# Optimization experiments

Measured on AMD Instinct MI355X. Metric: run time of the kernel, lower is better.

Reference implementation:

```python
import jax, jax.numpy as jnp
import numpy as np

# dims (match init_kwargs)
T, B, N, D_OB = 256, 32, 64, 4
D_MODEL = N * D_OB            # 256
D_PE = 16
D_T = D_MODEL + D_PE          # 272 transformer width
H = 8
DH = D_T // H                 # 34
L = 2
DFF = 1024
C = 2
MAX_LEN = T
F_IN = T * D_OB               # 1024, ObservationPropagation channels


def setup_inputs() -> dict:
    key = jax.random.key(0)
    ks = jax.random.split(key, 24)
    g = lambda k, shp: 0.02 * jax.random.normal(k, shp, dtype=jnp.float32)
    return {
        "x": jax.random.normal(ks[0], (T, B, N), dtype=jnp.float32),
        "times": jnp.sort(jax.random.uniform(ks[1], (T, B), dtype=jnp.float32) * MAX_LEN, axis=0),
        "lengths": jax.random.randint(ks[2], (B,), MAX_LEN // 2, MAX_LEN + 1),
        "R_u": g(ks[3], (1, N * D_OB)),
        "Wv1": g(ks[4], (F_IN, F_IN)), "bv1": g(ks[5], (F_IN,)),
        "Wv2": g(ks[6], (F_IN, F_IN)), "bv2": g(ks[7], (F_IN,)),
        "qkv_w": g(ks[8], (L, D_T, 3 * D_T)), "qkv_b": g(ks[9], (L, 3 * D_T)),
        "out_w": g(ks[10], (L, D_T, D_T)), "out_b": g(ks[11], (L, D_T)),
        "ln1_w": jnp.ones((L, D_T), jnp.float32), "ln1_b": jnp.zeros((L, D_T), jnp.float32),
        "ln2_w": jnp.ones((L, D_T), jnp.float32), "ln2_b": jnp.zeros((L, D_T), jnp.float32),
        "ffn_w1": g(ks[12], (L, D_T, DFF)), "ffn_b1": g(ks[13], (L, DFF)),
        "ffn_w2": g(ks[14], (L, DFF, D_T)), "ffn_b2": g(ks[15], (L, D_T)),
        "mlp_w1": g(ks[16], (D_T, D_T)), "mlp_b1": g(ks[17], (D_T,)),
        "mlp_w2": g(ks[18], (D_T, C)), "mlp_b2": g(ks[19], (C,)),
    }


def _pos_encode(times):
    # PositionalEncodingTF: timescales = max_len ** linspace(0,1,d_pe//2)
    scales = MAX_LEN ** np.linspace(0.0, 1.0, D_PE // 2)
    st = times[..., None] / jnp.asarray(scales, times.dtype)  # [T,B,8]
    return jnp.concatenate([jnp.sin(st), jnp.cos(st)], axis=-1)  # [T,B,16]


def _segment_softmax(w, seg, num_segments):
    m = jax.ops.segment_max(w, seg, num_segments=num_segments)
    e = jnp.exp(w - m[seg])
    s = jax.ops.segment_sum(e, seg, num_segments=num_segments)
    return e / s[seg]


def _ob_propagate(xn, src, tgt, edge_w, Wv, bv):
    """Batched ObservationPropagation (use_beta=False, decompose=False).
    xn: [B,N,F]; messages = relu(lin_value(x_src)) * softmax(edge_w per target);
    scatter-add at targets. Returns (out, pre-softmax alpha == edge_w)."""
    gamma = _segment_softmax(edge_w, tgt, N)              # [E]
    value = jax.nn.relu(xn @ Wv + bv)                     # [B,N,F] (linear commutes with gather)
    msg = value[:, src, :] * gamma[None, :, None]         # [B,E,F] -- dominant memory traffic
    out = jnp.zeros_like(xn).at[:, tgt, :].add(msg)       # segment-sum at target nodes
    return out, edge_w


def _ln(x, w, b):
    mu = jnp.mean(x, axis=-1, keepdims=True)
    var = jnp.mean((x - mu) ** 2, axis=-1, keepdims=True)
    return (x - mu) / jnp.sqrt(var + 1e-5) * w + b


def _encoder_layer(xt, key_pad, qkv_w, qkv_b, out_w, out_b, ln1_w, ln1_b, ln2_w, ln2_b, w1, b1, w2, b2):
    # xt: [T,B,D_T]; key_pad: [B,T] True = padded. Post-norm torch TransformerEncoderLayer, relu, no dropout.
    Tt, Bb, _ = xt.shape
    q, k, v = jnp.split(xt @ qkv_w + qkv_b, 3, axis=-1)
    to_h = lambda t: t.reshape(Tt, Bb, H, DH).transpose(1, 2, 0, 3)  # [B,H,T,dh]
    scores = jnp.einsum("bhqd,bhkd->bhqk", to_h(q), to_h(k)) / jnp.sqrt(jnp.asarray(DH, xt.dtype))
    scores = jnp.where(key_pad[:, None, None, :], -jnp.inf, scores)
    attn = jax.nn.softmax(scores, axis=-1)
    o = jnp.einsum("bhqk,bhkd->bhqd", attn, to_h(v)).transpose(2, 0, 1, 3).reshape(Tt, Bb, D_T)
    xt = _ln(xt + o @ out_w + out_b, ln1_w, ln1_b)
    ff = jax.nn.relu(xt @ w1 + b1) @ w2 + b2
    return _ln(xt + ff, ln2_w, ln2_b)


def _forward(x, times, lengths, R_u, Wv1, bv1, Wv2, bv2, qkv_w, qkv_b, out_w, out_b,
             ln1_w, ln1_b, ln2_w, ln2_b, ffn_w1, ffn_b1, ffn_w2, ffn_b2,
             mlp_w1, mlp_b1, mlp_w2, mlp_b2):
    Bb = x.shape[1]
    # observation embedding: repeat each sensor d_ob times, scale by R_u, relu
    h = jax.nn.relu(jnp.repeat(x, D_OB, axis=-1) * R_u)          # [T,B,N*d_ob]
    pe = _pos_encode(times)                                      # [T,B,16]
    key_pad = jnp.arange(T)[None, :] >= lengths[:, None]         # [B,T]
    # reshape to per-sensor node features: [B, N, T*d_ob]
    xn = h.reshape(T, Bb, N, D_OB).transpose(1, 2, 0, 3).reshape(Bb, N, F_IN)
    # dense all-pairs graph (global_structure = ones); torch.nonzero order is row-major
    src = jnp.repeat(jnp.arange(N), N)   # edge_index[0]
    tgt = jnp.tile(jnp.arange(N), N)     # edge_index[1] (aggregation index)
    ew = jnp.ones((N * N,), x.dtype)
    xn, ew2 = _ob_propagate(xn, src, tgt, ew, Wv1, bv1)
    xn, _ = _ob_propagate(xn, src, tgt, ew2, Wv2, bv2)
    out = xn.reshape(Bb, N, T, D_OB).transpose(2, 0, 1, 3).reshape(T, Bb, N * D_OB)
    out = jnp.concatenate([out, pe], axis=2)                     # [T,B,272]
    for l in range(L):
        out = _encoder_layer(out, key_pad, qkv_w[l], qkv_b[l], out_w[l], out_b[l],
                             ln1_w[l], ln1_b[l], ln2_w[l], ln2_b[l],
                             ffn_w1[l], ffn_b1[l], ffn_w2[l], ffn_b2[l])
    keep = (~key_pad).T[:, :, None].astype(out.dtype)            # [T,B,1]
    agg = jnp.sum(out * keep, axis=0) / (lengths[:, None].astype(out.dtype) + 1.0)
    hid = jax.nn.relu(agg @ mlp_w1 + mlp_b1)
    logits = hid @ mlp_w2 + mlp_b2
    return jax.nn.softmax(logits, axis=1)                        # [B,C]


def reference(x, times, lengths, R_u, Wv1, bv1, Wv2, bv2, qkv_w, qkv_b, out_w, out_b,
              ln1_w, ln1_b, ln2_w, ln2_b, ffn_w1, ffn_b1, ffn_w2, ffn_b2,
              mlp_w1, mlp_b1, mlp_w2, mlp_b2):
    return _forward(x, times, lengths, R_u, Wv1, bv1, Wv2, bv2, qkv_w, qkv_b, out_w, out_b,
                    ln1_w, ln1_b, ln2_w, ln2_b, ffn_w1, ffn_b1, ffn_w2, ffn_b2,
                    mlp_w1, mlp_b1, mlp_w2, mlp_b2)
```

## Files before the change

### kernel.cpp

```cpp
#include <hip/hip_runtime.h>
#include <math.h>

#define T_DIM 256
#define B_DIM 32
#define N_DIM 64
#define F_INF 1024
#define D_T 272
#define H_DIM 8
#define DH_DIM 34
#define DFF_DIM 1024

typedef unsigned int uint;
typedef short bf16x8 __attribute__((ext_vector_type(8)));
typedef float f32x4 __attribute__((ext_vector_type(4)));

__device__ __forceinline__ ushort f2bf(float f) {
    uint u = __float_as_uint(f);
    uint r = (u + 0x7fffu + ((u >> 16) & 1u)) >> 16;
    return (ushort)r;
}
__device__ __forceinline__ float bf2f(ushort u) {
    return __uint_as_float(((uint)u) << 16);
}

__global__ void xn_kernel(const float* __restrict__ x, const float* __restrict__ Ru,
                          ushort* __restrict__ xn) {
    int idx = blockIdx.x * blockDim.x + threadIdx.x;
    if (idx >= B_DIM * N_DIM * F_INF) return;
    int f = idx & 1023;
    int bn = idx >> 10;
    int n = bn & 63;
    int b = bn >> 6;
    int t = f >> 2;
    int d = f & 3;
    float v = x[(t * B_DIM + b) * N_DIM + n] * Ru[(n << 2) + d];
    xn[idx] = f2bf(fmaxf(v, 0.0f));
}

struct WT {
    int tstart[11];
    const float* src[10];
    ushort* dst[10];
    int K[10];
    int N[10];
    int ntn[10];
};
__global__ __launch_bounds__(256) void wconv_tiled(WT s) {
    int tile = blockIdx.x;
    int seg = 0;
    while (seg < 9 && tile >= s.tstart[seg + 1]) ++seg;
    int ti = tile - s.tstart[seg];
    int ntn = s.ntn[seg];
    int tk = ti / ntn, tn = ti - tk * ntn;
    int K = s.K[seg], N = s.N[seg];
    __shared__ float t[16][17];
    int ty = threadIdx.x >> 4, tx = threadIdx.x & 15;
    t[ty][tx] = s.src[seg][(size_t)(tk * 16 + ty) * N + tn * 16 + tx];
    __syncthreads();
    s.dst[seg][(size_t)(tn * 16 + ty) * K + tk * 16 + tx] = f2bf(t[tx][ty]);
}

template <int ACT, int OUT_MODE>
__global__ __launch_bounds__(256) void gemm_mfma(const ushort* __restrict__ A,
                                                 const ushort* __restrict__ Bt,
                                                 const float* __restrict__ bias,
                                                 void* __restrict__ Cout,
                                                 int M, int N, int K) {
    __shared__ ushort As[2][64 * 32];
    __shared__ ushort Bs[2][128 * 32];
    const int tid = threadIdx.x;
    const int m0 = blockIdx.y * 64;
    const int n0 = blockIdx.x * 128;
    const int w = tid >> 6, lane = tid & 63;
    const int wr = w >> 1, wc = w & 1;
    const int lr = lane & 15, lk = lane >> 4;

    const int nfull = K >> 5;
    const int ns = (K + 31) >> 5;

    const int ra = w * 16 + (lane >> 2);
    const int ca = (((lane & 3) ^ ((ra >> 1) & 3)) << 3);
    int gma = m0 + ra; if (gma > M - 1) gma = M - 1;
    const ushort* gA = &A[(size_t)gma * K + ca];
    const int rb0 = w * 32 + (lane >> 2);
    const int cb0 = (((lane & 3) ^ ((rb0 >> 1) & 3)) << 3);
    const int rb1 = rb0 + 16;
    const int cb1 = (((lane & 3) ^ ((rb1 >> 1) & 3)) << 3);
    int gnb0 = n0 + rb0; if (gnb0 > N - 1) gnb0 = N - 1;
    int gnb1 = n0 + rb1; if (gnb1 > N - 1) gnb1 = N - 1;
    const ushort* gB0 = &Bt[(size_t)gnb0 * K + cb0];
    const ushort* gB1 = &Bt[(size_t)gnb1 * K + cb1];

    f32x4 acc[2][4];
#pragma unroll
    for (int i = 0; i < 2; ++i)
#pragma unroll
        for (int j = 0; j < 4; ++j) acc[i][j] = (f32x4){0.f, 0.f, 0.f, 0.f};

    auto stage = [&](int buf, int s) {
        const int k0 = s << 5;
        if (s < nfull) {
            __builtin_amdgcn_global_load_lds(
                (const __attribute__((address_space(1))) void*)(gA + k0),
                (__attribute__((address_space(3))) void*)(&As[buf][w * 512]), 16, 0, 0);
            __builtin_amdgcn_global_load_lds(
                (const __attribute__((address_space(1))) void*)(gB0 + k0),
                (__attribute__((address_space(3))) void*)(&Bs[buf][w * 1024]), 16, 0, 0);
            __builtin_amdgcn_global_load_lds(
                (const __attribute__((address_space(1))) void*)(gB1 + k0),
                (__attribute__((address_space(3))) void*)(&Bs[buf][w * 1024 + 512]), 16, 0, 0);
        } else {
            {
                int r = tid >> 2, p = tid & 3;
                int g = p ^ ((r >> 1) & 3);
                int gm = m0 + r; if (gm > M - 1) gm = M - 1;
                ushort v[8];
#pragma unroll
                for (int e = 0; e < 8; ++e) {
                    int gk = k0 + g * 8 + e;
                    v[e] = (gk < K) ? A[(size_t)gm * K + gk] : (ushort)0;
                }
                *reinterpret_cast<uint4*>(&As[buf][r * 32 + p * 8]) =
                    *reinterpret_cast<uint4*>(v);
            }
#pragma unroll
            for (int rr = 0; rr < 2; ++rr) {
                int r = rr * 64 + (tid >> 2), p = tid & 3;
                int g = p ^ ((r >> 1) & 3);
                int gn = n0 + r; if (gn > N - 1) gn = N - 1;
                ushort v[8];
#pragma unroll
                for (int e = 0; e < 8; ++e) {
                    int gk = k0 + g * 8 + e;
                    v[e] = (gk < K) ? Bt[(size_t)gn * K + gk] : (ushort)0;
                }
                *reinterpret_cast<uint4*>(&Bs[buf][r * 32 + p * 8]) =
                    *reinterpret_cast<uint4*>(v);
            }
        }
    };

    stage(0, 0);
    asm volatile("s_waitcnt vmcnt(0) lgkmcnt(0)" ::: "memory");
    __builtin_amdgcn_sched_barrier(0);
    __builtin_amdgcn_s_barrier();
    __builtin_amdgcn_sched_barrier(0);

    int cur = 0;
    for (int s = 0; s < ns; ++s) {
        if (s + 1 < ns) stage(cur ^ 1, s + 1);

        bf16x8 af[2], bf[4];
#pragma unroll
        for (int mt = 0; mt < 2; ++mt) {
            int row = wr * 32 + mt * 16 + lr;
            int ch = lk ^ ((row >> 1) & 3);
            af[mt] = *reinterpret_cast<const bf16x8*>(&As[cur][row * 32 + ch * 8]);
        }
#pragma unroll
        for (int nt = 0; nt < 4; ++nt) {
            int row = wc * 64 + nt * 16 + lr;
            int ch = lk ^ ((row >> 1) & 3);
            bf[nt] = *reinterpret_cast<const bf16x8*>(&Bs[cur][row * 32 + ch * 8]);
        }
        __builtin_amdgcn_s_setprio(1);
#pragma unroll
        for (int mt = 0; mt < 2; ++mt)
#pragma unroll
            for (int nt = 0; nt < 4; ++nt)
                acc[mt][nt] = __builtin_amdgcn_mfma_f32_16x16x32_bf16(
                    af[mt], bf[nt], acc[mt][nt], 0, 0, 0);
        __builtin_amdgcn_s_setprio(0);

        if (s + 1 < ns) {
            asm volatile("s_waitcnt vmcnt(0) lgkmcnt(0)" ::: "memory");
            __builtin_amdgcn_sched_barrier(0);
            __builtin_amdgcn_s_barrier();
            __builtin_amdgcn_sched_barrier(0);
        }
        cur ^= 1;
    }

#pragma unroll
    for (int nt = 0; nt < 4; ++nt) {
        int col = n0 + wc * 64 + nt * 16 + lr;
        if (col >= N) continue;
        float bv = bias[col];
        int g = 0, dcol = 0;
        if (OUT_MODE == 2) { g = col / 34; dcol = col - g * 34; }
#pragma unroll
        for (int mt = 0; mt < 2; ++mt) {
#pragma unroll
            for (int r = 0; r < 4; ++r) {
                int row = m0 + wr * 32 + mt * 16 + lk * 4 + r;
                if (row >= M) continue;
                float v = acc[mt][nt][r] + bv;
                if (ACT == 1) v = fmaxf(v, 0.0f);
                if (OUT_MODE == 0)
                    ((float*)Cout)[(size_t)row * N + col] = v;
                else if (OUT_MODE == 1)
                    ((ushort*)Cout)[(size_t)row * N + col] = f2bf(v);
                else
                    ((ushort*)Cout)[(size_t)row * 960 + g * 40 + dcol] = f2bf(v);
            }
        }
    }
}

__global__ __launch_bounds__(256) void reduce_s1_kernel(const ushort* __restrict__ val1,
                                                        ushort* __restrict__ s1) {
    int idx = blockIdx.x * 256 + threadIdx.x;
    if (idx >= B_DIM * 128) return;
    int b = idx >> 7;
    int g0 = (idx & 127) << 3;
    const ushort* base = val1 + (size_t)(b << 6) * F_INF + g0;
    float s[8] = {0.f, 0.f, 0.f, 0.f, 0.f, 0.f, 0.f, 0.f};
    for (int n = 0; n < 64; ++n) {
        bf16x8 v = *reinterpret_cast<const bf16x8*>(base + (size_t)n * F_INF);
#pragma unroll
        for (int e = 0; e < 8; ++e) s[e] += bf2f((ushort)v[e]);
    }
    ushort o[8];
#pragma unroll
    for (int e = 0; e < 8; ++e) o[e] = f2bf(s[e] * (1.0f / 64.0f));
    *reinterpret_cast<uint4*>(&s1[(size_t)idx * 8]) = *reinterpret_cast<uint4*>(o);
}

__global__ void seq_kernel(const float* __restrict__ out2, const float* __restrict__ times,
                           ushort* __restrict__ seq) {
    int idx = blockIdx.x * blockDim.x + threadIdx.x;
    if (idx >= T_DIM * B_DIM * D_T) return;
    int c = idx % D_T;
    int tb = idx / D_T;
    float v;
    if (c < 256) {
        v = out2[(tb % B_DIM) * 1024 + ((tb / B_DIM) << 2) + (c & 3)];
    } else {
        int s = c - 256;
        int sc = (s < 8) ? s : s - 8;
        float arg = times[tb] * exp2f(-8.0f * (float)sc * (1.0f / 7.0f));
        v = (s < 8) ? sinf(arg) : cosf(arg);
    }
    seq[idx] = f2bf(v);
}

__global__ void pad_zero_kernel(uint* __restrict__ qkvb) {
    int idx = blockIdx.x * blockDim.x + threadIdx.x;
    if (idx >= T_DIM * B_DIM * 24 * 3) return;
    int row = idx / 72;
    int r = idx - row * 72;
    int g = r / 3, q = r - g * 3;
    qkvb[(size_t)row * 480 + g * 20 + 17 + q] = 0;
}

__global__ __launch_bounds__(256) void attn_mfma(const ushort* __restrict__ qkv,
                                                 const int* __restrict__ lengths,
                                                 ushort* __restrict__ attno) {
    const int b = blockIdx.x >> 3;
    const int h = blockIdx.x & 7;
    const int tid = threadIdx.x;
    const int w = tid >> 6, lane = tid & 63;
    const int lr = lane & 15, lk = lane >> 4;
    __shared__ ushort Ks[2][64 * 40];
    __shared__ ushort Vt[2][48 * 72];
    __shared__ ushort Ps[4][64 * 72];
    const int len = lengths[b];
    const float scale = 0.1714985851f;
    const bf16x8 zv = {0, 0, 0, 0, 0, 0, 0, 0};

    for (int i = tid; i < 2 * 8 * 72; i += 256) {
        int bb = i / 576;
        Vt[bb][40 * 72 + (i - bb * 576)] = 0;
    }

    const int srow0 = tid / 5, sch0 = tid - srow0 * 5;
    const int srow1 = (tid + 256) / 5, sch1 = (tid + 256) - srow1 * 5;
    const int sjp0 = (srow0 & 15) * 4 + (srow0 >> 4);
    const int sjp1 = (srow1 & 15) * 4 + (srow1 >> 4);
    const bool has1 = (tid < 64);
    bf16x8 kreg0, kreg1, vreg0, vreg1;

    auto LOADS = [&](int c) {
        const ushort* b0 = &qkv[(size_t)((c * 64 + srow0) * 32 + b) * 960 + h * 40];
        kreg0 = *reinterpret_cast<const bf16x8*>(b0 + 320 + sch0 * 8);
        vreg0 = *reinterpret_cast<const bf16x8*>(b0 + 640 + sch0 * 8);
        if (has1) {
            const ushort* b1 = &qkv[(size_t)((c * 64 + srow1) * 32 + b) * 960 + h * 40];
            kreg1 = *reinterpret_cast<const bf16x8*>(b1 + 320 + sch1 * 8);
            vreg1 = *reinterpret_cast<const bf16x8*>(b1 + 640 + sch1 * 8);
        }
    };
    auto WRITES = [&](int buf) {
        *reinterpret_cast<bf16x8*>(&Ks[buf][srow0 * 40 + sch0 * 8]) = kreg0;
#pragma unroll
        for (int e = 0; e < 8; ++e) Vt[buf][(sch0 * 8 + e) * 72 + sjp0] = (ushort)vreg0[e];
        if (has1) {
            *reinterpret_cast<bf16x8*>(&Ks[buf][srow1 * 40 + sch1 * 8]) = kreg1;
#pragma unroll
            for (int e = 0; e < 8; ++e) Vt[buf][(sch1 * 8 + e) * 72 + sjp1] = (ushort)vreg1[e];
        }
    };

    bf16x8 qf0[4], qf1[4];
#pragma unroll
    for (int it = 0; it < 4; ++it) {
        int t = w * 64 + it * 16 + lr;
        const ushort* qrow = &qkv[(size_t)(t * 32 + b) * 960 + h * 40];
        qf0[it] = *reinterpret_cast<const bf16x8*>(qrow + lk * 8);
        qf1[it] = (lk == 0) ? *reinterpret_cast<const bf16x8*>(qrow + 32) : zv;
    }

    f32x4 oacc[4][3];
#pragma unroll
    for (int it = 0; it < 4; ++it)
#pragma unroll
        for (int dt = 0; dt < 3; ++dt) oacc[it][dt] = (f32x4){0.f, 0.f, 0.f, 0.f};
    float m[4][4], l[4][4];
#pragma unroll
    for (int it = 0; it < 4; ++it)
#pragma unroll
        for (int r = 0; r < 4; ++r) { m[it][r] = -1e30f; l[it][r] = 0.f; }

    const int nchunks = (len + 63) >> 6;
    LOADS(0);
    WRITES(0);
    __syncthreads();

    int cur = 0;
    for (int c = 0; c < nchunks; ++c) {
        const bool pre = (c + 1 < nchunks);
        if (pre) LOADS(c + 1);

        bf16x8 kf0[4], kf1[4];
#pragma unroll
        for (int jt = 0; jt < 4; ++jt) {
            int j = jt * 16 + lr;
            kf0[jt] = *reinterpret_cast<const bf16x8*>(&Ks[cur][j * 40 + lk * 8]);
            kf1[jt] = (lk == 0) ? *reinterpret_cast<const bf16x8*>(&Ks[cur][j * 40 + 32]) : zv;
        }

        const bool tail = (c * 64 + 64 > len);
#pragma unroll
        for (int it = 0; it < 4; ++it) {
            f32x4 sacc[4];
#pragma unroll
            for (int jt = 0; jt < 4; ++jt) sacc[jt] = (f32x4){0.f, 0.f, 0.f, 0.f};
            __builtin_amdgcn_s_setprio(1);
#pragma unroll
            for (int jt = 0; jt < 4; ++jt) {
                sacc[jt] = __builtin_amdgcn_mfma_f32_16x16x32_bf16(qf0[it], kf0[jt],
                                                                   sacc[jt], 0, 0, 0);
                sacc[jt] = __builtin_amdgcn_mfma_f32_16x16x32_bf16(qf1[it], kf1[jt],
                                                                   sacc[jt], 0, 0, 0);
            }
            __builtin_amdgcn_s_setprio(0);
            float cm[4] = {-1e30f, -1e30f, -1e30f, -1e30f};
#pragma unroll
            for (int jt = 0; jt < 4; ++jt) {
                bool dead = tail && (c * 64 + jt * 16 + lr >= len);
#pragma unroll
                for (int r = 0; r < 4; ++r) {
                    float sv = dead ? -1e30f : sacc[jt][r];
                    sacc[jt][r] = sv;
                    cm[r] = fmaxf(cm[r], sv);
                }
            }
#pragma unroll
            for (int mask = 1; mask <= 8; mask <<= 1)
#pragma unroll
                for (int r = 0; r < 4; ++r) cm[r] = fmaxf(cm[r], __shfl_xor(cm[r], mask));
#pragma unroll
            for (int r = 0; r < 4; ++r) {
                float mn = fmaxf(m[it][r], cm[r]);
                float corr = __expf((m[it][r] - mn) * scale);
                m[it][r] = mn;
                l[it][r] *= corr;
#pragma unroll
                for (int dt = 0; dt < 3; ++dt) oacc[it][dt][r] *= corr;
            }
            float ls[4] = {0.f, 0.f, 0.f, 0.f};
#pragma unroll
            for (int jt = 0; jt < 4; ++jt)
#pragma unroll
                for (int r = 0; r < 4; ++r) {
                    float e = __expf((sacc[jt][r] - m[it][r]) * scale);
                    sacc[jt][r] = e;
                    ls[r] += e;
                }
#pragma unroll
            for (int mask = 1; mask <= 8; mask <<= 1)
#pragma unroll
                for (int r = 0; r < 4; ++r) ls[r] += __shfl_xor(ls[r], mask);
#pragma unroll
            for (int r = 0; r < 4; ++r) l[it][r] += ls[r];
#pragma unroll
            for (int r = 0; r < 4; ++r) {
                int i = it * 16 + lk * 4 + r;
                uint u0 = (uint)f2bf(sacc[0][r]) | ((uint)f2bf(sacc[1][r]) << 16);
                uint u1 = (uint)f2bf(sacc[2][r]) | ((uint)f2bf(sacc[3][r]) << 16);
                uint2 pk = make_uint2(u0, u1);
                *reinterpret_cast<uint2*>(&Ps[w][i * 72 + lr * 4]) = pk;
            }
        }

        bf16x8 vf[3][2], pf[4][2];
#pragma unroll
        for (int dt = 0; dt < 3; ++dt)
#pragma unroll
            for (int ks = 0; ks < 2; ++ks)
                vf[dt][ks] = *reinterpret_cast<const bf16x8*>(
                    &Vt[cur][(dt * 16 + lr) * 72 + ks * 32 + lk * 8]);
#pragma unroll
        for (int it = 0; it < 4; ++it)
#pragma unroll
            for (int ks = 0; ks < 2; ++ks)
                pf[it][ks] = *reinterpret_cast<const bf16x8*>(
                    &Ps[w][(it * 16 + lr) * 72 + ks * 32 + lk * 8]);
        __builtin_amdgcn_s_setprio(1);
#pragma unroll
        for (int it = 0; it < 4; ++it)
#pragma unroll
            for (int dt = 0; dt < 3; ++dt)
#pragma unroll
                for (int ks = 0; ks < 2; ++ks)
                    oacc[it][dt] = __builtin_amdgcn_mfma_f32_16x16x32_bf16(
                        pf[it][ks], vf[dt][ks], oacc[it][dt], 0, 0, 0);
        __builtin_amdgcn_s_setprio(0);

        if (pre) WRITES(cur ^ 1);
        __syncthreads();
        cur ^= 1;
    }

#pragma unroll
    for (int it = 0; it < 4; ++it)
#pragma unroll
        for (int r = 0; r < 4; ++r) {
            float inv = 1.0f / l[it][r];
            int t = w * 64 + it * 16 + lk * 4 + r;
            ushort* orow = &attno[(size_t)(t * 32 + b) * 272 + h * 34];
#pragma unroll
            for (int dt = 0; dt < 3; ++dt) {
                int d = dt * 16 + lr;
                if (d < 34) orow[d] = f2bf(oacc[it][dt][r] * inv);
            }
        }
}

__global__ __launch_bounds__(256) void ln_kernel(const ushort* __restrict__ X,
                                                 const float* __restrict__ Y,
                                                 const float* __restrict__ w,
                                                 const float* __restrict__ bsh,
                                                 ushort* __restrict__ out) {
    int row = blockIdx.x * 4 + (threadIdx.x >> 6);
    int lane = threadIdx.x & 63;
    const ushort* xr = X + (size_t)row * D_T;
    const float* yr = Y + (size_t)row * D_T;
    float v[5];
    float sum = 0.f, sumsq = 0.f;
#pragma unroll
    for (int k = 0; k < 5; ++k) {
        int c = lane + k * 64;
        float t = 0.f;
        if (c < D_T) t = bf2f(xr[c]) + yr[c];
        v[k] = t;
        sum += t;
        sumsq += t * t;
    }
#pragma unroll
    for (int off = 32; off; off >>= 1) {
        sum += __shfl_down(sum, off);
        sumsq += __shfl_down(sumsq, off);
    }
    sum = __shfl(sum, 0);
    sumsq = __shfl(sumsq, 0);
    float mu = sum * (1.0f / D_T);
    float var = sumsq * (1.0f / D_T) - mu * mu;
    float inv = 1.0f / sqrtf(var + 1e-5f);
    ushort* orow = out + (size_t)row * D_T;
#pragma unroll
    for (int k = 0; k < 5; ++k) {
        int c = lane + k * 64;
        if (c < D_T) orow[c] = f2bf((v[k] - mu) * inv * w[c] + bsh[c]);
    }
}

__global__ __launch_bounds__(256) void pool_partial(const ushort* __restrict__ seq,
                                                    const int* __restrict__ lengths,
                                                    float* __restrict__ partial) {
    const int chunk = blockIdx.x;
    const int b = blockIdx.y;
    const int tid = threadIdx.x;
    if (tid >= 136) return;
    const int len = lengths[b];
    float s0 = 0.f, s1 = 0.f;
    int t0 = chunk * 32;
    int tmax = len - t0;
    if (tmax > 32) tmax = 32;
#pragma unroll 4
    for (int r = 0; r < tmax; ++r) {
        uint u = *reinterpret_cast<const uint*>(
            &seq[(size_t)((t0 + r) * B_DIM + b) * D_T + tid * 2]);
        s0 += __uint_as_float(u << 16);
        s1 += __uint_as_float(u & 0xffff0000u);
    }
    float* p = &partial[(size_t)(chunk * B_DIM + b) * D_T + tid * 2];
    p[0] = s0;
    p[1] = s1;
}

__global__ __launch_bounds__(256) void head_kernel(const float* __restrict__ partial,
                                                   const int* __restrict__ lengths,
                                                   const float* __restrict__ w1,
                                                   const float* __restrict__ b1,
                                                   const float* __restrict__ w2,
                                                   const float* __restrict__ b2,
                                                   float* __restrict__ out) {
    const int b = blockIdx.x;
    const int tid = threadIdx.x;
    const int len = lengths[b];
    __shared__ float agg_s[D_T];
    __shared__ float hid[D_T];
    float inv = 1.0f / (float)(len + 1);
    for (int c = tid; c < D_T; c += 256) {
        float s = 0.f;
#pragma unroll
        for (int ch = 0; ch < 8; ++ch)
            s += partial[(size_t)(ch * B_DIM + b) * D_T + c];
        agg_s[c] = s * inv;
    }
    __syncthreads();
    for (int j = tid; j < D_T; j += 256) {
        float acc = b1[j];
        for (int k = 0; k < D_T; ++k) acc += agg_s[k] * w1[k * D_T + j];
        hid[j] = fmaxf(acc, 0.f);
    }
    __syncthreads();
    if (tid < 64) {
        float l0 = 0.f, l1 = 0.f;
        for (int k = tid; k < D_T; k += 64) {
            float hv = hid[k];
            l0 += hv * w2[k * 2 + 0];
            l1 += hv * w2[k * 2 + 1];
        }
#pragma unroll
        for (int off = 32; off; off >>= 1) {
            l0 += __shfl_down(l0, off);
            l1 += __shfl_down(l1, off);
        }
        if (tid == 0) {
            l0 += b2[0];
            l1 += b2[1];
            float mx = fmaxf(l0, l1);
            float e0 = expf(l0 - mx), e1 = expf(l1 - mx);
            float nrm = 1.0f / (e0 + e1);
            out[b * 2 + 0] = e0 * nrm;
            out[b * 2 + 1] = e1 * nrm;
        }
    }
}

extern "C" void kernel_launch(void* const* d_in, const int* in_sizes, int n_in,
                              void* d_out, int out_size, void* d_ws, size_t ws_size,
                              hipStream_t stream) {
    const float* x      = (const float*)d_in[0];
    const float* times  = (const float*)d_in[1];
    const int*   lens   = (const int*)d_in[2];
    const float* R_u    = (const float*)d_in[3];
    const float* Wv1    = (const float*)d_in[4];
    const float* bv1    = (const float*)d_in[5];
    const float* Wv2    = (const float*)d_in[6];
    const float* bv2    = (const float*)d_in[7];
    const float* qkv_w  = (const float*)d_in[8];
    const float* qkv_b  = (const float*)d_in[9];
    const float* out_w  = (const float*)d_in[10];
    const float* out_b  = (const float*)d_in[11];
    const float* ln1_w  = (const float*)d_in[12];
    const float* ln1_b  = (const float*)d_in[13];
    const float* ln2_w  = (const float*)d_in[14];
    const float* ln2_b  = (const float*)d_in[15];
    const float* ffn_w1 = (const float*)d_in[16];
    const float* ffn_b1 = (const float*)d_in[17];
    const float* ffn_w2 = (const float*)d_in[18];
    const float* ffn_b2 = (const float*)d_in[19];
    const float* mlp_w1 = (const float*)d_in[20];
    const float* mlp_b1 = (const float*)d_in[21];
    const float* mlp_w2 = (const float*)d_in[22];
    const float* mlp_b2 = (const float*)d_in[23];
    float* outp = (float*)d_out;

    char* base = (char*)d_ws;
    size_t used = 0;
    auto alloc = [&](size_t bytes) -> char* {
        char* p = base + used;
        used += (bytes + 255) & ~(size_t)255;
        return p;
    };
    const int TB = T_DIM * B_DIM;

    ushort* xn    = (ushort*)alloc((size_t)2048 * 1024 * 2);
    ushort* val1  = (ushort*)alloc((size_t)2048 * 1024 * 2);
    ushort* s1    = (ushort*)alloc((size_t)32 * 1024 * 2);
    float*  out2  = (float*) alloc((size_t)32 * 1024 * 4);
    ushort* seq   = (ushort*)alloc((size_t)TB * D_T * 2);
    ushort* qkvb  = (ushort*)alloc((size_t)TB * 960 * 2);
    ushort* attno = (ushort*)alloc((size_t)TB * D_T * 2);
    float*  tmp   = (float*) alloc((size_t)TB * D_T * 4);
    ushort* x1    = (ushort*)alloc((size_t)TB * D_T * 2);
    ushort* h1    = (ushort*)alloc((size_t)TB * DFF_DIM * 2);
    float*  ppart = (float*) alloc((size_t)8 * B_DIM * D_T * 4);
    ushort* wv1t  = (ushort*)alloc((size_t)1024 * 1024 * 2);
    ushort* wv2t  = (ushort*)alloc((size_t)1024 * 1024 * 2);
    ushort* qkvwt[2]; ushort* outwt[2]; ushort* f1wt[2]; ushort* f2wt[2];
    for (int l = 0; l < 2; ++l) {
        qkvwt[l] = (ushort*)alloc((size_t)272 * 816 * 2);
        outwt[l] = (ushort*)alloc((size_t)272 * 272 * 2);
        f1wt[l]  = (ushort*)alloc((size_t)272 * 1024 * 2);
        f2wt[l]  = (ushort*)alloc((size_t)1024 * 272 * 2);
    }
    if (used > ws_size) return;

    {
        WT segs;
        const float* srcs[10] = {Wv1, Wv2,
                                 qkv_w, out_w, ffn_w1, ffn_w2,
                                 qkv_w + (size_t)272 * 816, out_w + (size_t)272 * 272,
                                 ffn_w1 + (size_t)272 * 1024, ffn_w2 + (size_t)1024 * 272};
        ushort* dsts[10] = {wv1t, wv2t, qkvwt[0], outwt[0], f1wt[0], f2wt[0],
                            qkvwt[1], outwt[1], f1wt[1], f2wt[1]};
        int Ksz[10] = {1024, 1024, 272, 272, 272, 1024, 272, 272, 272, 1024};
        int Nsz[10] = {1024, 1024, 816, 272, 1024, 272, 816, 272, 1024, 272};
        int acc = 0;
        for (int i = 0; i < 10; ++i) {
            segs.tstart[i] = acc;
            segs.src[i] = srcs[i];
            segs.dst[i] = dsts[i];
            segs.K[i] = Ksz[i];
            segs.N[i] = Nsz[i];
            segs.ntn[i] = Nsz[i] / 16;
            acc += (Ksz[i] / 16) * (Nsz[i] / 16);
        }
        segs.tstart[10] = acc;
        wconv_tiled<<<acc, 256, 0, stream>>>(segs);
    }

    {
        int n = B_DIM * N_DIM * F_INF;
        xn_kernel<<<(n + 255) / 256, 256, 0, stream>>>(x, R_u, xn);
    }

    gemm_mfma<1, 1><<<dim3(8, 32), 256, 0, stream>>>(xn, wv1t, bv1, val1, 2048, 1024, 1024);
    reduce_s1_kernel<<<16, 256, 0, stream>>>(val1, s1);
    gemm_mfma<1, 0><<<dim3(8, 1), 256, 0, stream>>>(s1, wv2t, bv2, out2, 32, 1024, 1024);

    {
        int n = TB * D_T;
        seq_kernel<<<(n + 255) / 256, 256, 0, stream>>>(out2, times, seq);
    }

    {
        int n = TB * 24 * 3;
        pad_zero_kernel<<<(n + 255) / 256, 256, 0, stream>>>((uint*)qkvb);
    }

    for (int l = 0; l < 2; ++l) {
        const float* qb  = qkv_b + (size_t)l * 816;
        const float* ob  = out_b + (size_t)l * D_T;
        const float* l1w = ln1_w + (size_t)l * D_T;
        const float* l1b = ln1_b + (size_t)l * D_T;
        const float* l2w = ln2_w + (size_t)l * D_T;
        const float* l2b = ln2_b + (size_t)l * D_T;
        const float* f1b = ffn_b1 + (size_t)l * DFF_DIM;
        const float* f2b = ffn_b2 + (size_t)l * D_T;

        gemm_mfma<0, 2><<<dim3(7, 128), 256, 0, stream>>>(seq, qkvwt[l], qb, qkvb,
                                                          TB, 816, D_T);
        attn_mfma<<<B_DIM * H_DIM, 256, 0, stream>>>(qkvb, lens, attno);
        gemm_mfma<0, 0><<<dim3(3, 128), 256, 0, stream>>>(attno, outwt[l], ob, tmp,
                                                          TB, D_T, D_T);
        ln_kernel<<<TB / 4, 256, 0, stream>>>(seq, tmp, l1w, l1b, x1);
        gemm_mfma<1, 1><<<dim3(8, 128), 256, 0, stream>>>(x1, f1wt[l], f1b, h1,
                                                          TB, DFF_DIM, D_T);
        gemm_mfma<0, 0><<<dim3(3, 128), 256, 0, stream>>>(h1, f2wt[l], f2b, tmp,
                                                          TB, D_T, DFF_DIM);
        ln_kernel<<<TB / 4, 256, 0, stream>>>(x1, tmp, l2w, l2b, seq);
    }

    pool_partial<<<dim3(8, B_DIM), 256, 0, stream>>>(seq, lens, ppart);
    head_kernel<<<B_DIM, 256, 0, stream>>>(ppart, lens, mlp_w1, mlp_b1,
                                           mlp_w2, mlp_b2, outp);
}
```

Before: 336.3 us.

## Pad transformer K to 288, triple-buffer GEMM loads, split-K the small Wv2 GEMM

Activation and weight buffers with K=272 are padded to a stride of 288 with zeroed tails, so every K-step of the GEMM can use the async global_load_lds path and the slow scalar tail path is removed. The GEMM pipeline moves from double to triple buffering, prefetching two stages ahead with partial vmcnt waits. The M=32 Wv2 GEMM, which launched only 8 blocks, is split four ways along K into partial sums, followed by a reduce kernel that adds the bias and applies relu. The cost is more LDS per block, extra memsets and pad-initialisation work, and one more kernel launch.

```diff
diff --git a/kernel.cpp b/kernel.cpp
--- a/kernel.cpp
+++ b/kernel.cpp
@@ -6,6 +6,7 @@
 #define N_DIM 64
 #define F_INF 1024
 #define D_T 272
+#define D_TP 288
 #define H_DIM 8
 #define DH_DIM 34
 #define DFF_DIM 1024
@@ -43,6 +44,7 @@
     ushort* dst[10];
     int K[10];
     int N[10];
+    int Kp[10];
     int ntn[10];
 };
 __global__ __launch_bounds__(256) void wconv_tiled(WT s) {
@@ -52,12 +54,13 @@
     int ti = tile - s.tstart[seg];
     int ntn = s.ntn[seg];
     int tk = ti / ntn, tn = ti - tk * ntn;
-    int K = s.K[seg], N = s.N[seg];
+    int K = s.K[seg], N = s.N[seg], Kp = s.Kp[seg];
     __shared__ float t[16][17];
     int ty = threadIdx.x >> 4, tx = threadIdx.x & 15;
     t[ty][tx] = s.src[seg][(size_t)(tk * 16 + ty) * N + tn * 16 + tx];
     __syncthreads();
-    s.dst[seg][(size_t)(tn * 16 + ty) * K + tk * 16 + tx] = f2bf(t[tx][ty]);
+    s.dst[seg][(size_t)(tn * 16 + ty) * Kp + tk * 16 + tx] = f2bf(t[tx][ty]);
+    (void)K;
 }
 
 template <int ACT, int OUT_MODE>
@@ -65,31 +68,34 @@
                                                  const ushort* __restrict__ Bt,
                                                  const float* __restrict__ bias,
                                                  void* __restrict__ Cout,
-                                                 int M, int N, int K) {
-    __shared__ ushort As[2][64 * 32];
-    __shared__ ushort Bs[2][128 * 32];
+                                                 int M, int N, int K, int Kstride) {
+    __shared__ ushort As[3][64 * 32];
+    __shared__ ushort Bs[3][128 * 32];
     const int tid = threadIdx.x;
-    const int m0 = blockIdx.y * 64;
+    const int m0 = (OUT_MODE == 3) ? 0 : blockIdx.y * 64;
     const int n0 = blockIdx.x * 128;
+    if (OUT_MODE == 3) {
+        A += (size_t)blockIdx.y * K;
+        Bt += (size_t)blockIdx.y * K;
+    }
     const int w = tid >> 6, lane = tid & 63;
     const int wr = w >> 1, wc = w & 1;
     const int lr = lane & 15, lk = lane >> 4;
 
-    const int nfull = K >> 5;
-    const int ns = (K + 31) >> 5;
+    const int ns = K >> 5;
 
     const int ra = w * 16 + (lane >> 2);
     const int ca = (((lane & 3) ^ ((ra >> 1) & 3)) << 3);
     int gma = m0 + ra; if (gma > M - 1) gma = M - 1;
-    const ushort* gA = &A[(size_t)gma * K + ca];
+    const ushort* gA = &A[(size_t)gma * Kstride + ca];
     const int rb0 = w * 32 + (lane >> 2);
     const int cb0 = (((lane & 3) ^ ((rb0 >> 1) & 3)) << 3);
     const int rb1 = rb0 + 16;
     const int cb1 = (((lane & 3) ^ ((rb1 >> 1) & 3)) << 3);
     int gnb0 = n0 + rb0; if (gnb0 > N - 1) gnb0 = N - 1;
     int gnb1 = n0 + rb1; if (gnb1 > N - 1) gnb1 = N - 1;
-    const ushort* gB0 = &Bt[(size_t)gnb0 * K + cb0];
-    const ushort* gB1 = &Bt[(size_t)gnb1 * K + cb1];
+    const ushort* gB0 = &Bt[(size_t)gnb0 * Kstride + cb0];
+    const ushort* gB1 = &Bt[(size_t)gnb1 * Kstride + cb1];
 
     f32x4 acc[2][4];
 #pragma unroll
@@ -99,56 +105,28 @@
 
     auto stage = [&](int buf, int s) {
         const int k0 = s << 5;
-        if (s < nfull) {
-            __builtin_amdgcn_global_load_lds(
-                (const __attribute__((address_space(1))) void*)(gA + k0),
-                (__attribute__((address_space(3))) void*)(&As[buf][w * 512]), 16, 0, 0);
-            __builtin_amdgcn_global_load_lds(
-                (const __attribute__((address_space(1))) void*)(gB0 + k0),
-                (__attribute__((address_space(3))) void*)(&Bs[buf][w * 1024]), 16, 0, 0);
-            __builtin_amdgcn_global_load_lds(
-                (const __attribute__((address_space(1))) void*)(gB1 + k0),
-                (__attribute__((address_space(3))) void*)(&Bs[buf][w * 1024 + 512]), 16, 0, 0);
-        } else {
-            {
-                int r = tid >> 2, p = tid & 3;
-                int g = p ^ ((r >> 1) & 3);
-                int gm = m0 + r; if (gm > M - 1) gm = M - 1;
-                ushort v[8];
-#pragma unroll
-                for (int e = 0; e < 8; ++e) {
-                    int gk = k0 + g * 8 + e;
-                    v[e] = (gk < K) ? A[(size_t)gm * K + gk] : (ushort)0;
-                }
-                *reinterpret_cast<uint4*>(&As[buf][r * 32 + p * 8]) =
-                    *reinterpret_cast<uint4*>(v);
-            }
-#pragma unroll
-            for (int rr = 0; rr < 2; ++rr) {
-                int r = rr * 64 + (tid >> 2), p = tid & 3;
-                int g = p ^ ((r >> 1) & 3);
-                int gn = n0 + r; if (gn > N - 1) gn = N - 1;
-                ushort v[8];
-#pragma unroll
-                for (int e = 0; e < 8; ++e) {
-                    int gk = k0 + g * 8 + e;
-                    v[e] = (gk < K) ? Bt[(size_t)gn * K + gk] : (ushort)0;
-                }
-                *reinterpret_cast<uint4*>(&Bs[buf][r * 32 + p * 8]) =
-                    *reinterpret_cast<uint4*>(v);
-            }
-        }
+        __builtin_amdgcn_global_load_lds(
+            (const __attribute__((address_space(1))) void*)(gA + k0),
+            (__attribute__((address_space(3))) void*)(&As[buf][w * 512]), 16, 0, 0);
+        __builtin_amdgcn_global_load_lds(
+            (const __attribute__((address_space(1))) void*)(gB0 + k0),
+            (__attribute__((address_space(3))) void*)(&Bs[buf][w * 1024]), 16, 0, 0);
+        __builtin_amdgcn_global_load_lds(
+            (const __attribute__((address_space(1))) void*)(gB1 + k0),
+            (__attribute__((address_space(3))) void*)(&Bs[buf][w * 1024 + 512]), 16, 0, 0);
     };
 
     stage(0, 0);
-    asm volatile("s_waitcnt vmcnt(0) lgkmcnt(0)" ::: "memory");
+    stage(1, 1);
+    asm volatile("s_waitcnt vmcnt(3)" ::: "memory");
     __builtin_amdgcn_sched_barrier(0);
     __builtin_amdgcn_s_barrier();
     __builtin_amdgcn_sched_barrier(0);
 
     int cur = 0;
     for (int s = 0; s < ns; ++s) {
-        if (s + 1 < ns) stage(cur ^ 1, s + 1);
+        int stg = cur + 2; if (stg >= 3) stg -= 3;
+        if (s + 2 < ns) stage(stg, s + 2);
 
         bf16x8 af[2], bf[4];
 #pragma unroll
@@ -173,19 +151,22 @@
         __builtin_amdgcn_s_setprio(0);
 
         if (s + 1 < ns) {
-            asm volatile("s_waitcnt vmcnt(0) lgkmcnt(0)" ::: "memory");
+            if (s + 2 < ns)
+                asm volatile("s_waitcnt vmcnt(3)" ::: "memory");
+            else
+                asm volatile("s_waitcnt vmcnt(0)" ::: "memory");
             __builtin_amdgcn_sched_barrier(0);
             __builtin_amdgcn_s_barrier();
             __builtin_amdgcn_sched_barrier(0);
         }
-        cur ^= 1;
+        cur = (cur == 2) ? 0 : cur + 1;
     }
 
 #pragma unroll
     for (int nt = 0; nt < 4; ++nt) {
         int col = n0 + wc * 64 + nt * 16 + lr;
         if (col >= N) continue;
-        float bv = bias[col];
+        float bv = (OUT_MODE == 3) ? 0.f : bias[col];
         int g = 0, dcol = 0;
         if (OUT_MODE == 2) { g = col / 34; dcol = col - g * 34; }
 #pragma unroll
@@ -200,8 +181,10 @@
                     ((float*)Cout)[(size_t)row * N + col] = v;
                 else if (OUT_MODE == 1)
                     ((ushort*)Cout)[(size_t)row * N + col] = f2bf(v);
+                else if (OUT_MODE == 2)
+                    ((ushort*)Cout)[(size_t)row * 960 + g * 40 + dcol] = f2bf(v);
                 else
-                    ((ushort*)Cout)[(size_t)row * 960 + g * 40 + dcol] = f2bf(v);
+                    ((float*)Cout)[(size_t)(blockIdx.y * M + row) * N + col] = v;
             }
         }
     }
@@ -226,27 +209,50 @@
     *reinterpret_cast<uint4*>(&s1[(size_t)idx * 8]) = *reinterpret_cast<uint4*>(o);
 }
 
+__global__ __launch_bounds__(256) void reduce_p2_kernel(const float* __restrict__ part,
+                                                        const float* __restrict__ bv2,
+                                                        float* __restrict__ out2) {
+    int idx = blockIdx.x * 256 + threadIdx.x;
+    if (idx >= B_DIM * F_INF) return;
+    int g = idx & 1023;
+    float s = bv2[g];
+#pragma unroll
+    for (int ks = 0; ks < 4; ++ks) s += part[(size_t)ks * B_DIM * F_INF + idx];
+    out2[idx] = fmaxf(s, 0.f);
+}
+
 __global__ void seq_kernel(const float* __restrict__ out2, const float* __restrict__ times,
                            ushort* __restrict__ seq) {
     int idx = blockIdx.x * blockDim.x + threadIdx.x;
-    if (idx >= T_DIM * B_DIM * D_T) return;
-    int c = idx % D_T;
-    int tb = idx / D_T;
+    if (idx >= T_DIM * B_DIM * D_TP) return;
+    int c = idx % D_TP;
+    int tb = idx / D_TP;
     float v;
     if (c < 256) {
         v = out2[(tb % B_DIM) * 1024 + ((tb / B_DIM) << 2) + (c & 3)];
-    } else {
+    } else if (c < 272) {
         int s = c - 256;
         int sc = (s < 8) ? s : s - 8;
         float arg = times[tb] * exp2f(-8.0f * (float)sc * (1.0f / 7.0f));
         v = (s < 8) ? sinf(arg) : cosf(arg);
+    } else {
+        v = 0.f;
     }
     seq[idx] = f2bf(v);
 }
 
-__global__ void pad_zero_kernel(uint* __restrict__ qkvb) {
+__global__ void init_pads_kernel(uint* __restrict__ qkvb, uint* __restrict__ x1,
+                                 uint* __restrict__ attno) {
+    const int TB = T_DIM * B_DIM;
     int idx = blockIdx.x * blockDim.x + threadIdx.x;
-    if (idx >= T_DIM * B_DIM * 24 * 3) return;
+    if (idx < TB * 8) {
+        int row = idx >> 3, q = idx & 7;
+        x1[(size_t)row * 144 + 136 + q] = 0;
+        attno[(size_t)row * 144 + 136 + q] = 0;
+        return;
+    }
+    idx -= TB * 8;
+    if (idx >= TB * 72) return;
     int row = idx / 72;
     int r = idx - row * 72;
     int g = r / 3, q = r - g * 3;
@@ -438,7 +444,7 @@
         for (int r = 0; r < 4; ++r) {
             float inv = 1.0f / l[it][r];
             int t = w * 64 + it * 16 + lk * 4 + r;
-            ushort* orow = &attno[(size_t)(t * 32 + b) * 272 + h * 34];
+            ushort* orow = &attno[(size_t)(t * 32 + b) * D_TP + h * 34];
 #pragma unroll
             for (int dt = 0; dt < 3; ++dt) {
                 int d = dt * 16 + lr;
@@ -454,7 +460,7 @@
                                                  ushort* __restrict__ out) {
     int row = blockIdx.x * 4 + (threadIdx.x >> 6);
     int lane = threadIdx.x & 63;
-    const ushort* xr = X + (size_t)row * D_T;
+    const ushort* xr = X + (size_t)row * D_TP;
     const float* yr = Y + (size_t)row * D_T;
     float v[5];
     float sum = 0.f, sumsq = 0.f;
@@ -477,7 +483,7 @@
     float mu = sum * (1.0f / D_T);
     float var = sumsq * (1.0f / D_T) - mu * mu;
     float inv = 1.0f / sqrtf(var + 1e-5f);
-    ushort* orow = out + (size_t)row * D_T;
+    ushort* orow = out + (size_t)row * D_TP;
 #pragma unroll
     for (int k = 0; k < 5; ++k) {
         int c = lane + k * 64;
@@ -500,7 +506,7 @@
 #pragma unroll 4
     for (int r = 0; r < tmax; ++r) {
         uint u = *reinterpret_cast<const uint*>(
-            &seq[(size_t)((t0 + r) * B_DIM + b) * D_T + tid * 2]);
+            &seq[(size_t)((t0 + r) * B_DIM + b) * D_TP + tid * 2]);
         s0 += __uint_as_float(u << 16);
         s1 += __uint_as_float(u & 0xffff0000u);
     }
@@ -601,25 +607,31 @@
     ushort* xn    = (ushort*)alloc((size_t)2048 * 1024 * 2);
     ushort* val1  = (ushort*)alloc((size_t)2048 * 1024 * 2);
     ushort* s1    = (ushort*)alloc((size_t)32 * 1024 * 2);
+    float*  p2p   = (float*) alloc((size_t)4 * 32 * 1024 * 4);
     float*  out2  = (float*) alloc((size_t)32 * 1024 * 4);
-    ushort* seq   = (ushort*)alloc((size_t)TB * D_T * 2);
+    ushort* seq   = (ushort*)alloc((size_t)TB * D_TP * 2);
     ushort* qkvb  = (ushort*)alloc((size_t)TB * 960 * 2);
-    ushort* attno = (ushort*)alloc((size_t)TB * D_T * 2);
+    ushort* attno = (ushort*)alloc((size_t)TB * D_TP * 2);
     float*  tmp   = (float*) alloc((size_t)TB * D_T * 4);
-    ushort* x1    = (ushort*)alloc((size_t)TB * D_T * 2);
+    ushort* x1    = (ushort*)alloc((size_t)TB * D_TP * 2);
     ushort* h1    = (ushort*)alloc((size_t)TB * DFF_DIM * 2);
     float*  ppart = (float*) alloc((size_t)8 * B_DIM * D_T * 4);
     ushort* wv1t  = (ushort*)alloc((size_t)1024 * 1024 * 2);
     ushort* wv2t  = (ushort*)alloc((size_t)1024 * 1024 * 2);
     ushort* qkvwt[2]; ushort* outwt[2]; ushort* f1wt[2]; ushort* f2wt[2];
     for (int l = 0; l < 2; ++l) {
-        qkvwt[l] = (ushort*)alloc((size_t)272 * 816 * 2);
-        outwt[l] = (ushort*)alloc((size_t)272 * 272 * 2);
-        f1wt[l]  = (ushort*)alloc((size_t)272 * 1024 * 2);
-        f2wt[l]  = (ushort*)alloc((size_t)1024 * 272 * 2);
+        qkvwt[l] = (ushort*)alloc((size_t)816 * D_TP * 2);
+        outwt[l] = (ushort*)alloc((size_t)272 * D_TP * 2);
+        f1wt[l]  = (ushort*)alloc((size_t)1024 * D_TP * 2);
+        f2wt[l]  = (ushort*)alloc((size_t)272 * 1024 * 2);
     }
     if (used > ws_size) return;
 
+    for (int l = 0; l < 2; ++l) {
+        hipMemsetAsync(qkvwt[l], 0, (size_t)816 * D_TP * 2, stream);
+        hipMemsetAsync(outwt[l], 0, (size_t)272 * D_TP * 2, stream);
+        hipMemsetAsync(f1wt[l], 0, (size_t)1024 * D_TP * 2, stream);
+    }
     {
         WT segs;
         const float* srcs[10] = {Wv1, Wv2,
@@ -630,6 +642,7 @@
                             qkvwt[1], outwt[1], f1wt[1], f2wt[1]};
         int Ksz[10] = {1024, 1024, 272, 272, 272, 1024, 272, 272, 272, 1024};
         int Nsz[10] = {1024, 1024, 816, 272, 1024, 272, 816, 272, 1024, 272};
+        int Kpd[10] = {1024, 1024, D_TP, D_TP, D_TP, 1024, D_TP, D_TP, D_TP, 1024};
         int acc = 0;
         for (int i = 0; i < 10; ++i) {
             segs.tstart[i] = acc;
@@ -637,6 +650,7 @@
             segs.dst[i] = dsts[i];
             segs.K[i] = Ksz[i];
             segs.N[i] = Nsz[i];
+            segs.Kp[i] = Kpd[i];
             segs.ntn[i] = Nsz[i] / 16;
             acc += (Ksz[i] / 16) * (Nsz[i] / 16);
         }
@@ -649,18 +663,21 @@
         xn_kernel<<<(n + 255) / 256, 256, 0, stream>>>(x, R_u, xn);
     }
 
-    gemm_mfma<1, 1><<<dim3(8, 32), 256, 0, stream>>>(xn, wv1t, bv1, val1, 2048, 1024, 1024);
+    gemm_mfma<1, 1><<<dim3(8, 32), 256, 0, stream>>>(xn, wv1t, bv1, val1,
+                                                     2048, 1024, 1024, 1024);
     reduce_s1_kernel<<<16, 256, 0, stream>>>(val1, s1);
-    gemm_mfma<1, 0><<<dim3(8, 1), 256, 0, stream>>>(s1, wv2t, bv2, out2, 32, 1024, 1024);
+    gemm_mfma<0, 3><<<dim3(8, 4), 256, 0, stream>>>(s1, wv2t, nullptr, p2p,
+                                                    32, 1024, 256, 1024);
+    reduce_p2_kernel<<<128, 256, 0, stream>>>(p2p, bv2, out2);
 
     {
-        int n = TB * D_T;
+        int n = TB * D_TP;
         seq_kernel<<<(n + 255) / 256, 256, 0, stream>>>(out2, times, seq);
     }
-
     {
-        int n = TB * 24 * 3;
-        pad_zero_kernel<<<(n + 255) / 256, 256, 0, stream>>>((uint*)qkvb);
+        int n = TB * 8 + TB * 72;
+        init_pads_kernel<<<(n + 255) / 256, 256, 0, stream>>>((uint*)qkvb, (uint*)x1,
+                                                              (uint*)attno);
     }
 
     for (int l = 0; l < 2; ++l) {
@@ -674,15 +691,15 @@
         const float* f2b = ffn_b2 + (size_t)l * D_T;
 
         gemm_mfma<0, 2><<<dim3(7, 128), 256, 0, stream>>>(seq, qkvwt[l], qb, qkvb,
-                                                          TB, 816, D_T);
+                                                          TB, 816, D_TP, D_TP);
         attn_mfma<<<B_DIM * H_DIM, 256, 0, stream>>>(qkvb, lens, attno);
         gemm_mfma<0, 0><<<dim3(3, 128), 256, 0, stream>>>(attno, outwt[l], ob, tmp,
-                                                          TB, D_T, D_T);
+                                                          TB, D_T, D_TP, D_TP);
         ln_kernel<<<TB / 4, 256, 0, stream>>>(seq, tmp, l1w, l1b, x1);
         gemm_mfma<1, 1><<<dim3(8, 128), 256, 0, stream>>>(x1, f1wt[l], f1b, h1,
-                                                          TB, DFF_DIM, D_T);
+                                                          TB, DFF_DIM, D_TP, D_TP);
         gemm_mfma<0, 0><<<dim3(3, 128), 256, 0, stream>>>(h1, f2wt[l], f2b, tmp,
-                                                          TB, D_T, DFF_DIM);
+                                                          TB, D_T, 1024, 1024);
         ln_kernel<<<TB / 4, 256, 0, stream>>>(x1, tmp, l2w, l2b, seq);
     }
 
```

Measured after the change: 316.9 us. 1.06x faster.
